# Optimization experiments

Hardware: AMD Instinct MI355X
Metric: run time of the kernel (lower is better)

## Reference

```python
import jax, jax.numpy as jnp
import numpy as np

R = 4          # num_roles
L = 2          # num_layers
DIN = 128      # input/hidden feature dim
DOUT = 40     # output classes
N = 40000      # nodes
E = 480000     # edges


def setup_inputs() -> dict:
    key = jax.random.key(0)
    ks = jax.random.split(key, 12)
    x = jax.random.normal(ks[0], (N, R + DIN), dtype=jnp.float32)
    edge_index = jax.random.randint(ks[1], (2, E), 0, N, dtype=jnp.int64)
    s = 0.05
    Wm = jax.random.normal(ks[2], (L, R, DIN, DIN), dtype=jnp.float32) * s
    bm = jax.random.normal(ks[3], (L, R, DIN), dtype=jnp.float32) * s
    Wa = jax.random.normal(ks[4], (L, R, 2 * DIN, DIN), dtype=jnp.float32) * s
    ba = jax.random.normal(ks[5], (L, R, DIN), dtype=jnp.float32) * s
    W1 = jax.random.normal(ks[6], (DIN, DIN), dtype=jnp.float32) * s
    b1 = jax.random.normal(ks[7], (DIN,), dtype=jnp.float32) * s
    W2 = jax.random.normal(ks[8], (DIN, DOUT), dtype=jnp.float32) * s
    b2 = jax.random.normal(ks[9], (DOUT,), dtype=jnp.float32) * s
    return {"x": x, "edge_index": edge_index, "Wm": Wm, "bm": bm,
            "Wa": Wa, "ba": ba, "W1": W1, "b1": b1, "W2": W2, "b2": b2}


def _role_coef(roles):
    # Faithful to the original loop bug: linears[0] applied twice with roles[:,0],
    # linears[r] with roles[:,r] for r=1..R-2, linears[R-1] unused.
    return jnp.concatenate(
        [2.0 * roles[:, :1], roles[:, 1:R - 1], jnp.zeros_like(roles[:, :1])], axis=1)


def _graphsage_layer(xfull, src, dst, Wm_l, bm_l, Wa_l, ba_l):
    roles = xfull[:, :R]          # [N, R]
    feats = xfull[:, R:]          # [N, D]
    # --- message: gather source nodes, per-role linear + weighted sum, relu ---
    xr = roles[src]               # [E, R]
    xf = feats[src]               # [E, D]
    coef = _role_coef(xr)         # [E, R]
    lin = jnp.einsum('ei,rio->ero', xf, Wm_l) + bm_l[None]   # [E, R, O]
    msg = jax.nn.relu(jnp.einsum('er,ero->eo', coef, lin))    # [E, O]
    # --- aggregate: scatter-mean to target nodes ---
    ssum = jax.ops.segment_sum(msg, dst, num_segments=N)      # [N, O]
    cnt = jax.ops.segment_sum(jnp.ones((msg.shape[0], 1), msg.dtype), dst,
                              num_segments=N)                 # [N, 1]
    aggr = jnp.where(cnt > 0, ssum / jnp.maximum(cnt, 1.0), 0.0)
    # --- update: concat, per-role linear + weighted sum, relu, L2 normalize ---
    cat = jnp.concatenate([feats, aggr], axis=1)              # [N, D+O]
    coefn = _role_coef(roles)                                 # [N, R]
    lin2 = jnp.einsum('ni,rio->nro', cat, Wa_l) + ba_l[None]  # [N, R, O]
    out = jax.nn.relu(jnp.einsum('nr,nro->no', coefn, lin2))  # [N, O]
    norm = jnp.linalg.norm(out, axis=1, keepdims=True)
    return out / jnp.maximum(norm, 1e-12)


def reference(x, edge_index, Wm, bm, Wa, ba, W1, b1, W2, b2):
    src = edge_index[0]
    dst = edge_index[1]
    h = x
    for l in range(L):
        feats = _graphsage_layer(h, src, dst, Wm[l], bm[l], Wa[l], ba[l])
        feats = jax.nn.relu(feats)  # extra relu from GNNStack (dropout is identity in eval)
        h = jnp.concatenate([h[:, :R], feats], axis=1)
    z = h[:, R:]
    z = z @ W1 + b1               # post_mp linear 1 (dropout identity)
    logits = z @ W2 + b2          # post_mp linear 2
    return jax.nn.log_softmax(logits, axis=1)
```

## Files before the change

### kernel.cpp

```cpp
#include <hip/hip_runtime.h>
#include <hip/hip_fp16.h>

#define RN 4
#define XSTRIDE 132

typedef float    frag_cd __attribute__((ext_vector_type(4)));
typedef _Float16 frag_h  __attribute__((ext_vector_type(8)));

#define CW_M  (6 * 128 * 128)
#define CW_A  (6 * 128 * 256)
#define CW_1  (128 * 128)
#define CW_2  (48 * 128)
#define CW_TOT (CW_M + CW_A + CW_1 + CW_2)

__global__ void prep_kernel(
    const float* __restrict__ Wm, const float* __restrict__ Wa,
    const float* __restrict__ W1, const float* __restrict__ W2,
    _Float16* __restrict__ WmT, _Float16* __restrict__ WaT,
    _Float16* __restrict__ W1T, _Float16* __restrict__ W2T,
    const float* __restrict__ x, _Float16* __restrict__ X,
    const int* __restrict__ ei, int* __restrict__ cnt, int N, int E)
{
    int id = blockIdx.x * 256 + threadIdx.x;
    if (id < CW_M) {
        const int K = 128;
        int per = K * 128;
        int lr = id / per;  int l = lr / 3, r = lr - l * 3;
        int rem = id - lr * per;
        int k = rem >> 7, col = rem & 127;
        WmT[((size_t)lr * 128 + col) * K + k] =
            (_Float16)Wm[(((size_t)l * 4 + r) * K + k) * 128 + col];
        return;
    }
    id -= CW_M;
    if (id < CW_A) {
        const int K = 256;
        int per = K * 128;
        int lr = id / per;  int l = lr / 3, r = lr - l * 3;
        int rem = id - lr * per;
        int k = rem >> 7, col = rem & 127;
        WaT[((size_t)lr * 128 + col) * K + k] =
            (_Float16)Wa[(((size_t)l * 4 + r) * K + k) * 128 + col];
        return;
    }
    id -= CW_A;
    if (id < CW_1) {
        int col = id >> 7, k = id & 127;
        W1T[id] = (_Float16)W1[k * 128 + col];
        return;
    }
    id -= CW_1;
    if (id < CW_2) {
        int col = id >> 7, k = id & 127;
        W2T[id] = (_Float16)((col < 40) ? W2[k * 40 + col] : 0.0f);
        return;
    }
    id -= CW_2;
    if (id < N * 16) {
        int n = id >> 4, g = id & 15;
        const float4* src = (const float4*)(x + (size_t)n * XSTRIDE + RN + g * 8);
        float4 f0 = src[0], f1 = src[1];
        __half2 h0 = __float22half2_rn(make_float2(f0.x, f0.y));
        __half2 h1 = __float22half2_rn(make_float2(f0.z, f0.w));
        __half2 h2 = __float22half2_rn(make_float2(f1.x, f1.y));
        __half2 h3 = __float22half2_rn(make_float2(f1.z, f1.w));
        uint4 st; st.x = *(uint*)&h0; st.y = *(uint*)&h1;
        st.z = *(uint*)&h2; st.w = *(uint*)&h3;
        ((uint4*)X)[(size_t)n * 16 + g] = st;
        return;
    }
    id -= N * 16;
    if (id < E) atomicAdd(&cnt[ei[E + id]], 1);
}

__global__ void scanA(const int* __restrict__ cnt, int N, int* __restrict__ bsums) {
    __shared__ int s[256];
    int t = threadIdx.x, n = blockIdx.x * 256 + t;
    s[t] = (n < N) ? cnt[n] : 0;
    __syncthreads();
    for (int off = 128; off > 0; off >>= 1) {
        if (t < off) s[t] += s[t + off];
        __syncthreads();
    }
    if (t == 0) bsums[blockIdx.x] = s[0];
}

__global__ void scanC(const int* __restrict__ cnt, int N, int nb,
                      const int* __restrict__ bsums, int* __restrict__ offs) {
    __shared__ int s[256];
    __shared__ int basebuf[256];
    int t = threadIdx.x, n = blockIdx.x * 256 + t;
    int bid = blockIdx.x;
    basebuf[t] = (t < bid && t < nb) ? bsums[t] : 0;
    __syncthreads();
    for (int off = 128; off > 0; off >>= 1) {
        if (t < off) basebuf[t] += basebuf[t + off];
        __syncthreads();
    }
    int base = basebuf[0];
    int v = (n < N) ? cnt[n] : 0;
    s[t] = v; __syncthreads();
    for (int off = 1; off < 256; off <<= 1) {
        int add = (t >= off) ? s[t - off] : 0;
        __syncthreads();
        s[t] += add;
        __syncthreads();
    }
    if (n < N) {
        offs[n] = base + s[t] - v;
        if (n == N - 1) offs[N] = base + s[t];
    }
}

__global__ void fill_kernel(const int* __restrict__ ei, int E,
                            const int* __restrict__ offs, int* __restrict__ fc,
                            int* __restrict__ csr) {
    int e = blockIdx.x * 256 + threadIdx.x;
    if (e < E) {
        int dst = ei[E + e];
        int p = offs[dst] + atomicAdd(&fc[dst], 1);
        csr[p] = ei[e];
    }
}

__global__ __launch_bounds__(256) void agg_kernel(
    const int* __restrict__ csr, const int* __restrict__ offs,
    const _Float16* __restrict__ Mb, _Float16* __restrict__ S, int N)
{
    int node = blockIdx.x * 16 + (threadIdx.x >> 4);
    int lane = threadIdx.x & 15;
    if (node >= N) return;
    int lo = offs[node], hi = offs[node + 1];
    const uint4* M4 = (const uint4*)Mb;
    float a[8];
    #pragma unroll
    for (int i = 0; i < 8; ++i) a[i] = 0.0f;
    int e = lo;
    for (; e + 3 < hi; e += 4) {
        #pragma unroll
        for (int j = 0; j < 4; ++j) {
            uint4 u = M4[(size_t)csr[e + j] * 16 + lane];
            float2 f0 = __half22float2(*(const __half2*)&u.x);
            float2 f1 = __half22float2(*(const __half2*)&u.y);
            float2 f2 = __half22float2(*(const __half2*)&u.z);
            float2 f3 = __half22float2(*(const __half2*)&u.w);
            a[0] += f0.x; a[1] += f0.y; a[2] += f1.x; a[3] += f1.y;
            a[4] += f2.x; a[5] += f2.y; a[6] += f3.x; a[7] += f3.y;
        }
    }
    for (; e < hi; ++e) {
        uint4 u = M4[(size_t)csr[e] * 16 + lane];
        float2 f0 = __half22float2(*(const __half2*)&u.x);
        float2 f1 = __half22float2(*(const __half2*)&u.y);
        float2 f2 = __half22float2(*(const __half2*)&u.z);
        float2 f3 = __half22float2(*(const __half2*)&u.w);
        a[0] += f0.x; a[1] += f0.y; a[2] += f1.x; a[3] += f1.y;
        a[4] += f2.x; a[5] += f2.y; a[6] += f3.x; a[7] += f3.y;
    }
    float inv = (hi > lo) ? 1.0f / (float)(hi - lo) : 0.0f;
    __half2 h0 = __float22half2_rn(make_float2(a[0] * inv, a[1] * inv));
    __half2 h1 = __float22half2_rn(make_float2(a[2] * inv, a[3] * inv));
    __half2 h2 = __float22half2_rn(make_float2(a[4] * inv, a[5] * inv));
    __half2 h3 = __float22half2_rn(make_float2(a[6] * inv, a[7] * inv));
    uint4 st; st.x = *(uint*)&h0; st.y = *(uint*)&h1;
    st.z = *(uint*)&h2; st.w = *(uint*)&h3;
    ((uint4*)S)[(size_t)node * 16 + lane] = st;
}

__global__ __launch_bounds__(256) void msg_kernel(
    const float* __restrict__ x,
    const _Float16* __restrict__ Fp,
    const _Float16* __restrict__ W,
    const float* __restrict__ bias,
    _Float16* __restrict__ out)
{
    __shared__ float cc[64][3];

    const int tid = threadIdx.x;
    const int n0 = blockIdx.x * 64;
    const int lane = tid & 63;
    const int wv = tid >> 6;
    const int q = lane >> 4;
    const int lb = lane & 15;
    const int w32 = wv * 32;

    if (tid < 64) {
        const float* xr = x + (size_t)(n0 + tid) * XSTRIDE;
        cc[tid][0] = 2.0f * xr[0];
        cc[tid][1] = xr[1];
        cc[tid][2] = xr[2];
    }
    __syncthreads();

    _Float16 ch16[4][3];
    #pragma unroll
    for (int nt = 0; nt < 4; ++nt)
        #pragma unroll
        for (int r = 0; r < 3; ++r)
            ch16[nt][r] = (_Float16)cc[nt * 16 + lb][r];

    frag_cd acc[4][2];
    #pragma unroll
    for (int nt = 0; nt < 4; ++nt)
        #pragma unroll
        for (int ct = 0; ct < 2; ++ct)
            acc[nt][ct] = (frag_cd){0.f, 0.f, 0.f, 0.f};

    size_t wrow[3][2];
    #pragma unroll
    for (int r = 0; r < 3; ++r)
        #pragma unroll
        for (int ct = 0; ct < 2; ++ct)
            wrow[r][ct] = ((size_t)(r * 128 + w32 + ct * 16 + lb)) * 128 + q * 8;

    size_t arow[4];
    #pragma unroll
    for (int nt = 0; nt < 4; ++nt)
        arow[nt] = (size_t)(n0 + nt * 16 + lb) * 128 + q * 8;

    frag_h aF[4][4], bF[4][6];
    #pragma unroll
    for (int c = 0; c < 4; ++c) {
        #pragma unroll
        for (int nt = 0; nt < 4; ++nt)
            aF[c][nt] = *(const frag_h*)(Fp + arow[nt] + c * 32);
        #pragma unroll
        for (int r = 0; r < 3; ++r)
            #pragma unroll
            for (int ct = 0; ct < 2; ++ct)
                bF[c][r * 2 + ct] = *(const frag_h*)(W + wrow[r][ct] + c * 32);
    }
    #pragma unroll
    for (int c = 0; c < 4; ++c)
        #pragma unroll
        for (int r = 0; r < 3; ++r)
            #pragma unroll
            for (int nt = 0; nt < 4; ++nt) {
                frag_h sa = aF[c][nt] * ch16[nt][r];
                #pragma unroll
                for (int ct = 0; ct < 2; ++ct)
                    acc[nt][ct] = __builtin_amdgcn_mfma_f32_16x16x32_f16(
                        sa, bF[c][r * 2 + ct], acc[nt][ct], 0, 0, 0);
            }

    #pragma unroll
    for (int ct = 0; ct < 2; ++ct) {
        int col = w32 + ct * 16 + lb;
        float b0 = bias[col], b1 = bias[128 + col], b2 = bias[256 + col];
        #pragma unroll
        for (int nt = 0; nt < 4; ++nt)
            #pragma unroll
            for (int rg = 0; rg < 4; ++rg) {
                int row = nt * 16 + q * 4 + rg;
                float v = acc[nt][ct][rg]
                        + cc[row][0] * b0 + cc[row][1] * b1 + cc[row][2] * b2;
                out[(size_t)(n0 + row) * 128 + col] = (_Float16)fmaxf(v, 0.0f);
            }
    }
}

#define UPDATE_PHASE_A(Fp, Sp, Wa_, ba_)                                      \
    _Float16 ch16[4][3];                                                      \
    _Pragma("unroll")                                                         \
    for (int nt = 0; nt < 4; ++nt)                                            \
        _Pragma("unroll")                                                     \
        for (int r = 0; r < 3; ++r)                                           \
            ch16[nt][r] = (_Float16)cc[nt * 16 + lb][r];                      \
    frag_cd acc[4][2];                                                        \
    _Pragma("unroll")                                                         \
    for (int nt = 0; nt < 4; ++nt)                                            \
        _Pragma("unroll")                                                     \
        for (int ct = 0; ct < 2; ++ct)                                        \
            acc[nt][ct] = (frag_cd){0.f, 0.f, 0.f, 0.f};                      \
    size_t wrow[3][2];                                                        \
    _Pragma("unroll")                                                         \
    for (int r = 0; r < 3; ++r)                                               \
        _Pragma("unroll")                                                     \
        for (int ct = 0; ct < 2; ++ct)                                        \
            wrow[r][ct] = ((size_t)(r * 128 + w32 + ct * 16 + lb)) * 256 + q * 8; \
    size_t arow[4];                                                           \
    _Pragma("unroll")                                                         \
    for (int nt = 0; nt < 4; ++nt)                                            \
        arow[nt] = (size_t)(n0 + nt * 16 + lb) * 128 + q * 8;                 \
    {                                                                         \
        frag_h aF[3][4], bF[3][6];                                            \
        auto loadChunk = [&](int c, int buf) {                                \
            const _Float16* ap; int kofs;                                     \
            if (c < 4) { ap = (Fp); kofs = c * 32; }                          \
            else       { ap = (Sp); kofs = (c - 4) * 32; }                    \
            _Pragma("unroll")                                                 \
            for (int nt = 0; nt < 4; ++nt)                                    \
                aF[buf][nt] = *(const frag_h*)(ap + arow[nt] + kofs);         \
            _Pragma("unroll")                                                 \
            for (int r = 0; r < 3; ++r)                                       \
                _Pragma("unroll")                                             \
                for (int ct = 0; ct < 2; ++ct)                                \
                    bF[buf][r * 2 + ct] = *(const frag_h*)((Wa_) + wrow[r][ct] + c * 32); \
        };                                                                    \
        loadChunk(0, 0);                                                      \
        loadChunk(1, 1);                                                      \
        _Pragma("unroll")                                                     \
        for (int ch = 0; ch < 8; ++ch) {                                      \
            if (ch + 2 < 8) loadChunk(ch + 2, (ch + 2) % 3);                  \
            const int cur = ch % 3;                                           \
            _Pragma("unroll")                                                 \
            for (int r = 0; r < 3; ++r)                                       \
                _Pragma("unroll")                                             \
                for (int nt = 0; nt < 4; ++nt) {                              \
                    frag_h sa = aF[cur][nt] * ch16[nt][r];                    \
                    _Pragma("unroll")                                         \
                    for (int ct = 0; ct < 2; ++ct)                            \
                        acc[nt][ct] = __builtin_amdgcn_mfma_f32_16x16x32_f16( \
                            sa, bF[cur][r * 2 + ct], acc[nt][ct], 0, 0, 0);   \
                }                                                             \
        }                                                                     \
    }                                                                         \
    float vv[4][2][4];                                                        \
    _Pragma("unroll")                                                         \
    for (int ct = 0; ct < 2; ++ct) {                                          \
        int col = w32 + ct * 16 + lb;                                         \
        float b0 = (ba_)[col], b1 = (ba_)[128 + col], b2 = (ba_)[256 + col];  \
        _Pragma("unroll")                                                     \
        for (int nt = 0; nt < 4; ++nt)                                        \
            _Pragma("unroll")                                                 \
            for (int rg = 0; rg < 4; ++rg) {                                  \
                int row = nt * 16 + q * 4 + rg;                               \
                float v = acc[nt][ct][rg]                                     \
                        + cc[row][0] * b0 + cc[row][1] * b1 + cc[row][2] * b2;\
                vv[nt][ct][rg] = fmaxf(v, 0.0f);                              \
            }                                                                 \
    }                                                                         \
    _Pragma("unroll")                                                         \
    for (int nt = 0; nt < 4; ++nt)                                            \
        _Pragma("unroll")                                                     \
        for (int rg = 0; rg < 4; ++rg) {                                      \
            float ss = vv[nt][0][rg] * vv[nt][0][rg] + vv[nt][1][rg] * vv[nt][1][rg]; \
            _Pragma("unroll")                                                 \
            for (int m = 1; m < 16; m <<= 1) ss += __shfl_xor(ss, m, 64);     \
            if (lb == 0) red[nt * 16 + q * 4 + rg][wv] = ss;                  \
        }                                                                     \
    __syncthreads();                                                          \
    _Pragma("unroll")                                                         \
    for (int nt = 0; nt < 4; ++nt)                                            \
        _Pragma("unroll")                                                     \
        for (int rg = 0; rg < 4; ++rg) {                                      \
            int row = nt * 16 + q * 4 + rg;                                   \
            float t = red[row][0] + red[row][1] + red[row][2] + red[row][3];  \
            float inv = 1.0f / fmaxf(sqrtf(t), 1e-12f);                       \
            _Pragma("unroll")                                                 \
            for (int ct = 0; ct < 2; ++ct)                                    \
                Fs[row][w32 + ct * 16 + lb] = (_Float16)(vv[nt][ct][rg] * inv); \
        }                                                                     \
    __syncthreads();

__global__ __launch_bounds__(256) void fused_upd_msg(
    const float* __restrict__ x,
    const _Float16* __restrict__ Fp, const _Float16* __restrict__ Sp,
    const _Float16* __restrict__ Wa_, const float* __restrict__ ba_,
    const _Float16* __restrict__ Wm2, const float* __restrict__ bm2,
    _Float16* __restrict__ F1, _Float16* __restrict__ Mb)
{
    __shared__ float cc[64][3];
    __shared__ float red[64][4];
    __shared__ _Float16 Fs[64][136];

    const int tid = threadIdx.x;
    const int n0 = blockIdx.x * 64;
    const int lane = tid & 63;
    const int wv = tid >> 6;
    const int q = lane >> 4;
    const int lb = lane & 15;
    const int w32 = wv * 32;

    if (tid < 64) {
        const float* xr = x + (size_t)(n0 + tid) * XSTRIDE;
        cc[tid][0] = 2.0f * xr[0];
        cc[tid][1] = xr[1];
        cc[tid][2] = xr[2];
    }
    __syncthreads();

    UPDATE_PHASE_A(Fp, Sp, Wa_, ba_)

    #pragma unroll
    for (int i = 0; i < 4; ++i) {
        int idx = i * 256 + tid;
        int row = idx >> 4, g = idx & 15;
        ((uint4*)F1)[(size_t)(n0 + row) * 16 + g] = *(const uint4*)&Fs[row][g * 8];
    }

    frag_cd a2[4][2];
    #pragma unroll
    for (int nt = 0; nt < 4; ++nt)
        #pragma unroll
        for (int ct = 0; ct < 2; ++ct)
            a2[nt][ct] = (frag_cd){0.f, 0.f, 0.f, 0.f};

    frag_h bB[4][6];
    #pragma unroll
    for (int c = 0; c < 4; ++c)
        #pragma unroll
        for (int r = 0; r < 3; ++r)
            #pragma unroll
            for (int ct = 0; ct < 2; ++ct)
                bB[c][r * 2 + ct] = *(const frag_h*)(
                    Wm2 + ((size_t)(r * 128 + w32 + ct * 16 + lb)) * 128 + c * 32 + q * 8);

    #pragma unroll
    for (int c = 0; c < 4; ++c) {
        frag_h aM[4];
        #pragma unroll
        for (int nt = 0; nt < 4; ++nt)
            aM[nt] = *(const frag_h*)&Fs[nt * 16 + lb][c * 32 + q * 8];
        #pragma unroll
        for (int r = 0; r < 3; ++r)
            #pragma unroll
            for (int nt = 0; nt < 4; ++nt) {
                frag_h sa = aM[nt] * ch16[nt][r];
                #pragma unroll
                for (int ct = 0; ct < 2; ++ct)
                    a2[nt][ct] = __builtin_amdgcn_mfma_f32_16x16x32_f16(
                        sa, bB[c][r * 2 + ct], a2[nt][ct], 0, 0, 0);
            }
    }

    #pragma unroll
    for (int ct = 0; ct < 2; ++ct) {
        int col = w32 + ct * 16 + lb;
        float b0 = bm2[col], b1 = bm2[128 + col], b2 = bm2[256 + col];
        #pragma unroll
        for (int nt = 0; nt < 4; ++nt)
            #pragma unroll
            for (int rg = 0; rg < 4; ++rg) {
                int row = nt * 16 + q * 4 + rg;
                float v = a2[nt][ct][rg]
                        + cc[row][0] * b0 + cc[row][1] * b1 + cc[row][2] * b2;
                Mb[(size_t)(n0 + row) * 128 + col] = (_Float16)fmaxf(v, 0.0f);
            }
    }
}

__global__ __launch_bounds__(256) void fused_upd_final(
    const float* __restrict__ x,
    const _Float16* __restrict__ Fp, const _Float16* __restrict__ Sp,
    const _Float16* __restrict__ Wa_, const float* __restrict__ ba_,
    const _Float16* __restrict__ W1T, const float* __restrict__ b1,
    const _Float16* __restrict__ W2T, const float* __restrict__ b2,
    float* __restrict__ out)
{
    __shared__ float cc[64][3];
    __shared__ float red[64][4];
    __shared__ _Float16 Fs[64][136];
    __shared__ _Float16 Z[64][136];

    const int tid = threadIdx.x;
    const int n0 = blockIdx.x * 64;
    const int lane = tid & 63;
    const int wv = tid >> 6;
    const int q = lane >> 4;
    const int lb = lane & 15;
    const int w32 = wv * 32;

    if (tid < 64) {
        const float* xr = x + (size_t)(n0 + tid) * XSTRIDE;
        cc[tid][0] = 2.0f * xr[0];
        cc[tid][1] = xr[1];
        cc[tid][2] = xr[2];
    }
    __syncthreads();

    UPDATE_PHASE_A(Fp, Sp, Wa_, ba_)

    frag_cd az[4][2];
    #pragma unroll
    for (int nt = 0; nt < 4; ++nt)
        #pragma unroll
        for (int ct = 0; ct < 2; ++ct)
            az[nt][ct] = (frag_cd){0.f, 0.f, 0.f, 0.f};

    frag_h bZ[4][2];
    #pragma unroll
    for (int c = 0; c < 4; ++c)
        #pragma unroll
        for (int ct = 0; ct < 2; ++ct)
            bZ[c][ct] = *(const frag_h*)(
                W1T + (size_t)(w32 + ct * 16 + lb) * 128 + c * 32 + q * 8);

    #pragma unroll
    for (int c = 0; c < 4; ++c) {
        frag_h aZ[4];
        #pragma unroll
        for (int nt = 0; nt < 4; ++nt)
            aZ[nt] = *(const frag_h*)&Fs[nt * 16 + lb][c * 32 + q * 8];
        #pragma unroll
        for (int ct = 0; ct < 2; ++ct)
            #pragma unroll
            for (int nt = 0; nt < 4; ++nt)
                az[nt][ct] = __builtin_amdgcn_mfma_f32_16x16x32_f16(
                    aZ[nt], bZ[c][ct], az[nt][ct], 0, 0, 0);
    }
    #pragma unroll
    for (int ct = 0; ct < 2; ++ct) {
        int col = w32 + ct * 16 + lb;
        float bb = b1[col];
        #pragma unroll
        for (int nt = 0; nt < 4; ++nt)
            #pragma unroll
            for (int rg = 0; rg < 4; ++rg)
                Z[nt * 16 + q * 4 + rg][col] = (_Float16)(az[nt][ct][rg] + bb);
    }
    __syncthreads();

    frag_cd a2[3];
    #pragma unroll
    for (int ct = 0; ct < 3; ++ct) a2[ct] = (frag_cd){0.f, 0.f, 0.f, 0.f};
    #pragma unroll
    for (int ch = 0; ch < 4; ++ch) {
        frag_h zF = *(const frag_h*)&Z[wv * 16 + lb][ch * 32 + q * 8];
        #pragma unroll
        for (int ct = 0; ct < 3; ++ct) {
            frag_h bF = *(const frag_h*)(W2T + (size_t)(ct * 16 + lb) * 128 + ch * 32 + q * 8);
            a2[ct] = __builtin_amdgcn_mfma_f32_16x16x32_f16(zF, bF, a2[ct], 0, 0, 0);
        }
    }

    float lg[3][4];
    #pragma unroll
    for (int ct = 0; ct < 3; ++ct) {
        int col = ct * 16 + lb;
        bool valid = col < 40;
        float bb = valid ? b2[col] : -1e30f;
        #pragma unroll
        for (int rg = 0; rg < 4; ++rg)
            lg[ct][rg] = valid ? (a2[ct][rg] + bb) : -1e30f;
    }
    #pragma unroll
    for (int rg = 0; rg < 4; ++rg) {
        float mx = fmaxf(fmaxf(lg[0][rg], lg[1][rg]), lg[2][rg]);
        #pragma unroll
        for (int m = 1; m < 16; m <<= 1) mx = fmaxf(mx, __shfl_xor(mx, m, 64));
        float sm = __expf(lg[0][rg] - mx) + __expf(lg[1][rg] - mx) + __expf(lg[2][rg] - mx);
        #pragma unroll
        for (int m = 1; m < 16; m <<= 1) sm += __shfl_xor(sm, m, 64);
        float ls = mx + __logf(sm);
        int row = n0 + wv * 16 + q * 4 + rg;
        #pragma unroll
        for (int ct = 0; ct < 3; ++ct) {
            int col = ct * 16 + lb;
            if (col < 40) out[(size_t)row * 40 + col] = lg[ct][rg] - ls;
        }
    }
}

extern "C" void kernel_launch(void* const* d_in, const int* in_sizes, int n_in,
                              void* d_out, int out_size, void* d_ws, size_t ws_size,
                              hipStream_t stream) {
    const float* x  = (const float*)d_in[0];
    const int*   ei = (const int*)d_in[1];
    const float* Wm = (const float*)d_in[2];
    const float* bm = (const float*)d_in[3];
    const float* Wa = (const float*)d_in[4];
    const float* ba = (const float*)d_in[5];
    const float* W1 = (const float*)d_in[6];
    const float* b1 = (const float*)d_in[7];
    const float* W2 = (const float*)d_in[8];
    const float* b2 = (const float*)d_in[9];
    float* out = (float*)d_out;

    const int N = in_sizes[0] / XSTRIDE;
    const int E = in_sizes[1] / 2;
    const int NB = (N + 255) / 256;
    const size_t P = (size_t)N * 128;

    _Float16* Mb  = (_Float16*)d_ws;
    _Float16* X   = Mb + P;
    _Float16* S   = X + P;
    _Float16* F1  = S + P;
    _Float16* WmT = F1 + P;
    _Float16* WaT = WmT + CW_M;
    _Float16* W1T = WaT + CW_A;
    _Float16* W2T = W1T + CW_1;
    int* cnt   = (int*)(W2T + CW_2);
    int* fc    = cnt + N;
    int* offs  = fc + N;
    int* csr   = offs + N + 1;
    int* bsums = csr + E;

    hipMemsetAsync(cnt, 0, (size_t)2 * N * sizeof(int), stream);
    const int prep_total = CW_TOT + N * 16 + E;
    prep_kernel<<<(prep_total + 255) / 256, 256, 0, stream>>>(
        Wm, Wa, W1, W2, WmT, WaT, W1T, W2T, x, X, ei, cnt, N, E);

    scanA<<<NB, 256, 0, stream>>>(cnt, N, bsums);
    scanC<<<NB, 256, 0, stream>>>(cnt, N, NB, bsums, offs);
    fill_kernel<<<(E + 255) / 256, 256, 0, stream>>>(ei, E, offs, fc, csr);

    const int gblk = N / 64;
    const int ablk = (N + 15) / 16;

    msg_kernel<<<gblk, 256, 0, stream>>>(x, X, WmT, bm, Mb);
    agg_kernel<<<ablk, 256, 0, stream>>>(csr, offs, Mb, S, N);
    fused_upd_msg<<<gblk, 256, 0, stream>>>(
        x, X, S, WaT, ba,
        WmT + (size_t)3 * 128 * 128, bm + (size_t)4 * 128, F1, Mb);
    agg_kernel<<<ablk, 256, 0, stream>>>(csr, offs, Mb, S, N);
    fused_upd_final<<<gblk, 256, 0, stream>>>(
        x, F1, S, WaT + (size_t)3 * 128 * 256, ba + (size_t)4 * 128,
        W1T, b1, W2T, b2, out);
}
```

Before: 281.0 us.

## Stage activation tiles in LDS once per block instead of per-wave global loads

The message and update kernels now cooperatively copy each block's 64-row activation tile (features and aggregated sums) into shared memory with coalesced 16-byte loads. Each of the four waves then reads its A fragments from LDS, double-buffered one chunk ahead, rather than every wave re-reading the same rows from global memory. In the final kernel the Z buffer reuses the staged tile's LDS. The goal is fewer redundant global loads; the cost is higher LDS usage per block (about 52 KB in the update kernels), which may reduce occupancy.

```diff
diff --git a/kernel.cpp b/kernel.cpp
--- a/kernel.cpp
+++ b/kernel.cpp
@@ -167,6 +167,15 @@
     ((uint4*)S)[(size_t)node * 16 + lane] = st;
 }
 
+#define STAGE_TILE(dst, src, n0, tid)                                         \
+    _Pragma("unroll")                                                         \
+    for (int i_ = 0; i_ < 4; ++i_) {                                          \
+        int idx_ = i_ * 256 + (tid);                                          \
+        int row_ = idx_ >> 4, g_ = idx_ & 15;                                 \
+        *(uint4*)&(dst)[row_][g_ * 8] =                                       \
+            ((const uint4*)(src))[((size_t)((n0) + row_)) * 16 + g_];         \
+    }
+
 __global__ __launch_bounds__(256) void msg_kernel(
     const float* __restrict__ x,
     const _Float16* __restrict__ Fp,
@@ -174,6 +183,7 @@
     const float* __restrict__ bias,
     _Float16* __restrict__ out)
 {
+    __shared__ _Float16 As[64][136];
     __shared__ float cc[64][3];
 
     const int tid = threadIdx.x;
@@ -190,6 +200,7 @@
         cc[tid][1] = xr[1];
         cc[tid][2] = xr[2];
     }
+    STAGE_TILE(As, Fp, n0, tid)
     __syncthreads();
 
     _Float16 ch16[4][3];
@@ -206,42 +217,39 @@
         for (int ct = 0; ct < 2; ++ct)
             acc[nt][ct] = (frag_cd){0.f, 0.f, 0.f, 0.f};
 
-    size_t wrow[3][2];
-    #pragma unroll
-    for (int r = 0; r < 3; ++r)
-        #pragma unroll
-        for (int ct = 0; ct < 2; ++ct)
-            wrow[r][ct] = ((size_t)(r * 128 + w32 + ct * 16 + lb)) * 128 + q * 8;
-
-    size_t arow[4];
+    frag_h bF[4][6];
+    #pragma unroll
+    for (int c = 0; c < 4; ++c)
+        #pragma unroll
+        for (int r = 0; r < 3; ++r)
+            #pragma unroll
+            for (int ct = 0; ct < 2; ++ct)
+                bF[c][r * 2 + ct] = *(const frag_h*)(
+                    W + ((size_t)(r * 128 + w32 + ct * 16 + lb)) * 128 + c * 32 + q * 8);
+
+    frag_h aL[2][4];
     #pragma unroll
     for (int nt = 0; nt < 4; ++nt)
-        arow[nt] = (size_t)(n0 + nt * 16 + lb) * 128 + q * 8;
-
-    frag_h aF[4][4], bF[4][6];
+        aL[0][nt] = *(const frag_h*)&As[nt * 16 + lb][q * 8];
+
     #pragma unroll
     for (int c = 0; c < 4; ++c) {
-        #pragma unroll
-        for (int nt = 0; nt < 4; ++nt)
-            aF[c][nt] = *(const frag_h*)(Fp + arow[nt] + c * 32);
+        if (c + 1 < 4) {
+            #pragma unroll
+            for (int nt = 0; nt < 4; ++nt)
+                aL[(c + 1) & 1][nt] = *(const frag_h*)&As[nt * 16 + lb][(c + 1) * 32 + q * 8];
+        }
         #pragma unroll
         for (int r = 0; r < 3; ++r)
             #pragma unroll
-            for (int ct = 0; ct < 2; ++ct)
-                bF[c][r * 2 + ct] = *(const frag_h*)(W + wrow[r][ct] + c * 32);
-    }
-    #pragma unroll
-    for (int c = 0; c < 4; ++c)
-        #pragma unroll
-        for (int r = 0; r < 3; ++r)
-            #pragma unroll
             for (int nt = 0; nt < 4; ++nt) {
-                frag_h sa = aF[c][nt] * ch16[nt][r];
+                frag_h sa = aL[c & 1][nt] * ch16[nt][r];
                 #pragma unroll
                 for (int ct = 0; ct < 2; ++ct)
                     acc[nt][ct] = __builtin_amdgcn_mfma_f32_16x16x32_f16(
                         sa, bF[c][r * 2 + ct], acc[nt][ct], 0, 0, 0);
             }
+    }
 
     #pragma unroll
     for (int ct = 0; ct < 2; ++ct) {
@@ -259,7 +267,7 @@
     }
 }
 
-#define UPDATE_PHASE_A(Fp, Sp, Wa_, ba_)                                      \
+#define UPDATE_PHASE_A_LDS(Wa_, ba_)                                          \
     _Float16 ch16[4][3];                                                      \
     _Pragma("unroll")                                                         \
     for (int nt = 0; nt < 4; ++nt)                                            \
@@ -278,36 +286,38 @@
         _Pragma("unroll")                                                     \
         for (int ct = 0; ct < 2; ++ct)                                        \
             wrow[r][ct] = ((size_t)(r * 128 + w32 + ct * 16 + lb)) * 256 + q * 8; \
-    size_t arow[4];                                                           \
-    _Pragma("unroll")                                                         \
-    for (int nt = 0; nt < 4; ++nt)                                            \
-        arow[nt] = (size_t)(n0 + nt * 16 + lb) * 128 + q * 8;                 \
     {                                                                         \
-        frag_h aF[3][4], bF[3][6];                                            \
-        auto loadChunk = [&](int c, int buf) {                                \
-            const _Float16* ap; int kofs;                                     \
-            if (c < 4) { ap = (Fp); kofs = c * 32; }                          \
-            else       { ap = (Sp); kofs = (c - 4) * 32; }                    \
-            _Pragma("unroll")                                                 \
-            for (int nt = 0; nt < 4; ++nt)                                    \
-                aF[buf][nt] = *(const frag_h*)(ap + arow[nt] + kofs);         \
+        frag_h bF[3][6];                                                      \
+        auto loadB = [&](int c, int buf) {                                    \
             _Pragma("unroll")                                                 \
             for (int r = 0; r < 3; ++r)                                       \
                 _Pragma("unroll")                                             \
                 for (int ct = 0; ct < 2; ++ct)                                \
                     bF[buf][r * 2 + ct] = *(const frag_h*)((Wa_) + wrow[r][ct] + c * 32); \
         };                                                                    \
-        loadChunk(0, 0);                                                      \
-        loadChunk(1, 1);                                                      \
+        loadB(0, 0);                                                          \
+        loadB(1, 1);                                                          \
+        frag_h aL[2][4];                                                      \
+        _Pragma("unroll")                                                     \
+        for (int nt = 0; nt < 4; ++nt)                                        \
+            aL[0][nt] = *(const frag_h*)&As[nt * 16 + lb][q * 8];             \
         _Pragma("unroll")                                                     \
         for (int ch = 0; ch < 8; ++ch) {                                      \
-            if (ch + 2 < 8) loadChunk(ch + 2, (ch + 2) % 3);                  \
+            if (ch + 2 < 8) loadB(ch + 2, (ch + 2) % 3);                      \
+            if (ch + 1 < 8) {                                                 \
+                const int c1 = ch + 1;                                        \
+                _Pragma("unroll")                                             \
+                for (int nt = 0; nt < 4; ++nt)                                \
+                    aL[c1 & 1][nt] = (c1 < 4)                                 \
+                        ? *(const frag_h*)&As[nt * 16 + lb][c1 * 32 + q * 8]  \
+                        : *(const frag_h*)&Ss[nt * 16 + lb][(c1 - 4) * 32 + q * 8]; \
+            }                                                                 \
             const int cur = ch % 3;                                           \
             _Pragma("unroll")                                                 \
             for (int r = 0; r < 3; ++r)                                       \
                 _Pragma("unroll")                                             \
                 for (int nt = 0; nt < 4; ++nt) {                              \
-                    frag_h sa = aF[cur][nt] * ch16[nt][r];                    \
+                    frag_h sa = aL[ch & 1][nt] * ch16[nt][r];                 \
                     _Pragma("unroll")                                         \
                     for (int ct = 0; ct < 2; ++ct)                            \
                         acc[nt][ct] = __builtin_amdgcn_mfma_f32_16x16x32_f16( \
@@ -360,9 +370,11 @@
     const _Float16* __restrict__ Wm2, const float* __restrict__ bm2,
     _Float16* __restrict__ F1, _Float16* __restrict__ Mb)
 {
+    __shared__ _Float16 As[64][136];
+    __shared__ _Float16 Ss[64][136];
+    __shared__ _Float16 Fs[64][136];
     __shared__ float cc[64][3];
     __shared__ float red[64][4];
-    __shared__ _Float16 Fs[64][136];
 
     const int tid = threadIdx.x;
     const int n0 = blockIdx.x * 64;
@@ -378,9 +390,11 @@
         cc[tid][1] = xr[1];
         cc[tid][2] = xr[2];
     }
+    STAGE_TILE(As, Fp, n0, tid)
+    STAGE_TILE(Ss, Sp, n0, tid)
     __syncthreads();
 
-    UPDATE_PHASE_A(Fp, Sp, Wa_, ba_)
+    UPDATE_PHASE_A_LDS(Wa_, ba_)
 
     #pragma unroll
     for (int i = 0; i < 4; ++i) {
@@ -448,10 +462,11 @@
     const _Float16* __restrict__ W2T, const float* __restrict__ b2,
     float* __restrict__ out)
 {
+    __shared__ _Float16 As[64][136];
+    __shared__ _Float16 Ss[64][136];
+    __shared__ _Float16 Fs[64][136];
     __shared__ float cc[64][3];
     __shared__ float red[64][4];
-    __shared__ _Float16 Fs[64][136];
-    __shared__ _Float16 Z[64][136];
 
     const int tid = threadIdx.x;
     const int n0 = blockIdx.x * 64;
@@ -467,9 +482,11 @@
         cc[tid][1] = xr[1];
         cc[tid][2] = xr[2];
     }
+    STAGE_TILE(As, Fp, n0, tid)
+    STAGE_TILE(Ss, Sp, n0, tid)
     __syncthreads();
 
-    UPDATE_PHASE_A(Fp, Sp, Wa_, ba_)
+    UPDATE_PHASE_A_LDS(Wa_, ba_)
 
     frag_cd az[4][2];
     #pragma unroll
@@ -507,7 +524,7 @@
         for (int nt = 0; nt < 4; ++nt)
             #pragma unroll
             for (int rg = 0; rg < 4; ++rg)
-                Z[nt * 16 + q * 4 + rg][col] = (_Float16)(az[nt][ct][rg] + bb);
+                As[nt * 16 + q * 4 + rg][col] = (_Float16)(az[nt][ct][rg] + bb);
     }
     __syncthreads();
 
@@ -516,7 +533,7 @@
     for (int ct = 0; ct < 3; ++ct) a2[ct] = (frag_cd){0.f, 0.f, 0.f, 0.f};
     #pragma unroll
     for (int ch = 0; ch < 4; ++ch) {
-        frag_h zF = *(const frag_h*)&Z[wv * 16 + lb][ch * 32 + q * 8];
+        frag_h zF = *(const frag_h*)&As[wv * 16 + lb][ch * 32 + q * 8];
         #pragma unroll
         for (int ct = 0; ct < 3; ++ct) {
             frag_h bF = *(const frag_h*)(W2T + (size_t)(ct * 16 + lb) * 128 + ch * 32 + q * 8);
```

After: 270.4 us. 3.8% less time.
